# Kernel tuning notes

Hardware: AMD Instinct MI355X
Metric: run time of the kernel (lower is better)

Reference implementation:

```python
import jax, jax.numpy as jnp
import numpy as np

HIDDEN_DIM = 2048
NUM_HEADS = 16
HEAD_DIM = HIDDEN_DIM // NUM_HEADS


def setup_inputs() -> dict:
    key = jax.random.key(0)
    ks = jax.random.split(key, 5)
    B, S, D = 1, 4096, HIDDEN_DIM
    scale = 1.0 / np.sqrt(D)
    x = jax.random.normal(ks[0], (B, S, D), dtype=jnp.float32)
    w_q = jax.random.normal(ks[1], (D, D), dtype=jnp.float32) * scale
    w_k = jax.random.normal(ks[2], (D, D), dtype=jnp.float32) * scale
    w_v = jax.random.normal(ks[3], (D, D), dtype=jnp.float32) * scale
    w_o = jax.random.normal(ks[4], (D, D), dtype=jnp.float32) * scale
    return {"x": x, "w_q": w_q, "w_k": w_k, "w_v": w_v, "w_o": w_o, "causal": 1}


def reference(x, w_q, w_k, w_v, w_o, causal):
    B, S, D = x.shape
    H, Dh = NUM_HEADS, HEAD_DIM
    sm_scale = 1.0 / np.sqrt(Dh)

    # projections (x @ W.T)
    q = jnp.einsum('bsd,ed->bse', x, w_q).reshape(B, S, H, Dh).transpose(0, 2, 1, 3)
    k = jnp.einsum('bsd,ed->bse', x, w_k).reshape(B, S, H, Dh).transpose(0, 2, 1, 3)
    v = jnp.einsum('bsd,ed->bse', x, w_v).reshape(B, S, H, Dh).transpose(0, 2, 1, 3)

    # attention scores [B, H, S, S]; flash online-softmax == standard softmax
    scores = jnp.einsum('bhqd,bhkd->bhqk', q, k) * sm_scale
    if causal:
        qpos = jnp.arange(S)[:, None]
        kpos = jnp.arange(S)[None, :]
        scores = jnp.where(qpos >= kpos, scores, -jnp.inf)
    probs = jax.nn.softmax(scores, axis=-1)
    o = jnp.einsum('bhqk,bhkd->bhqd', probs, v)  # [B, H, S, Dh]
    o = o.transpose(0, 2, 1, 3).reshape(B, S, D)
    return jnp.einsum('bsd,ed->bse', o, w_o)
```

## Files before the change

### kernel.cpp

```cpp
#include <hip/hip_runtime.h>
#include <stdint.h>

typedef __bf16 bf16_t;
typedef __bf16 bf16x8 __attribute__((ext_vector_type(8)));
typedef __bf16 bf16x4 __attribute__((ext_vector_type(4)));
typedef float  f32x4  __attribute__((ext_vector_type(4)));

static constexpr int S  = 4096;
static constexpr int D  = 2048;
static constexpr int H  = 16;
static constexpr int DH = 128;

__device__ __forceinline__ bf16x8 ld8(const bf16_t* p) { return *(const bf16x8*)p; }
__device__ __forceinline__ bf16x8 ld8c(const float* p) {
  const f32x4 a = *(const f32x4*)p;
  const f32x4 b = *(const f32x4*)(p + 4);
  bf16x8 r;
  r[0] = (bf16_t)a[0]; r[1] = (bf16_t)a[1]; r[2] = (bf16_t)a[2]; r[3] = (bf16_t)a[3];
  r[4] = (bf16_t)b[0]; r[5] = (bf16_t)b[1]; r[6] = (bf16_t)b[2]; r[7] = (bf16_t)b[3];
  return r;
}

__device__ __forceinline__ void async_ld16(const bf16_t* g, bf16_t* lds) {
  __builtin_amdgcn_global_load_lds(
      (const __attribute__((address_space(1))) uint32_t*)g,
      (__attribute__((address_space(3))) uint32_t*)lds, 16, 0, 0);
}

__global__ __launch_bounds__(256) void cvt_kernel(
    const float* __restrict__ x,  const float* __restrict__ wq,
    const float* __restrict__ wk, const float* __restrict__ wv,
    const float* __restrict__ wo,
    bf16_t* __restrict__ xb,  bf16_t* __restrict__ wqb,
    bf16_t* __restrict__ wkb, bf16_t* __restrict__ wvb,
    bf16_t* __restrict__ wob) {
  const int z = blockIdx.z;
  const float* src; bf16_t* dst; size_t off = 0;
  if      (z == 0) { src = x;  dst = xb;  off = 0; }
  else if (z == 1) { src = x;  dst = xb;  off = 4194304; }
  else if (z == 2) { src = wq; dst = wqb; }
  else if (z == 3) { src = wk; dst = wkb; }
  else if (z == 4) { src = wv; dst = wvb; }
  else             { src = wo; dst = wob; }
  const size_t i = off + ((size_t)blockIdx.x * 256 + threadIdx.x) * 8;
  *(bf16x8*)(dst + i) = ld8c(src + i);
}

template <typename TC, bool TR>
__device__ __forceinline__ void gemm_async(const bf16_t* __restrict__ A,
                                           const bf16_t* __restrict__ W,
                                           TC* __restrict__ C) {
  constexpr int K  = D;
  constexpr int BK = 32;
  __shared__ __align__(16) bf16_t Ash[128 * BK];
  __shared__ __align__(16) bf16_t Bsh[128 * BK];
  const int tid = threadIdx.x;
  const int w = tid >> 6, lane = tid & 63;
  const int c = lane & 15, g = lane >> 4;
  const int wm = w >> 1, wn = w & 1;
  const int rowBase = blockIdx.y * 128;
  const int colBase = blockIdx.x * 128;

  f32x4 acc[4][4] = {};

  for (int k0 = 0; k0 < K; k0 += BK) {
    __syncthreads();
    #pragma unroll
    for (int r = 0; r < 2; ++r) {
      const int cid = r * 256 + tid;
      const int row = cid >> 2, q = cid & 3;
      async_ld16(A + (size_t)(rowBase + row) * K + k0 + q * 8,
                 Ash + r * 2048 + w * 512);
      async_ld16(W + (size_t)(colBase + row) * K + k0 + q * 8,
                 Bsh + r * 2048 + w * 512);
    }
    __syncthreads();

    bf16x8 af[4], bf[4];
    #pragma unroll
    for (int i = 0; i < 4; ++i) af[i] = ld8(Ash + (wm * 64 + i * 16 + c) * BK + g * 8);
    #pragma unroll
    for (int j = 0; j < 4; ++j) bf[j] = ld8(Bsh + (wn * 64 + j * 16 + c) * BK + g * 8);
    #pragma unroll
    for (int i = 0; i < 4; ++i)
      #pragma unroll
      for (int j = 0; j < 4; ++j)
        acc[i][j] = __builtin_amdgcn_mfma_f32_16x16x32_bf16(af[i], bf[j], acc[i][j], 0, 0, 0);
  }

  #pragma unroll
  for (int i = 0; i < 4; ++i)
    #pragma unroll
    for (int j = 0; j < 4; ++j) {
      if (TR) {
        const int col  = colBase + wn * 64 + j * 16 + c;
        const int row0 = rowBase + wm * 64 + i * 16 + g * 4;
        bf16x4 v;
        #pragma unroll
        for (int r = 0; r < 4; ++r) v[r] = (bf16_t)acc[i][j][r];
        *(bf16x4*)((bf16_t*)C + (size_t)col * S + row0) = v;
      } else {
        #pragma unroll
        for (int r = 0; r < 4; ++r) {
          const int row = rowBase + wm * 64 + i * 16 + g * 4 + r;
          const int col = colBase + wn * 64 + j * 16 + c;
          C[(size_t)row * D + col] = (TC)acc[i][j][r];
        }
      }
    }
}

__global__ __launch_bounds__(256) void qkv_gemm_bf16(
    const bf16_t* __restrict__ X,
    const bf16_t* __restrict__ Wq, const bf16_t* __restrict__ Wk,
    const bf16_t* __restrict__ Wv,
    bf16_t* __restrict__ Qo, bf16_t* __restrict__ Ko, bf16_t* __restrict__ VTo) {
  if (blockIdx.z == 0)      gemm_async<bf16_t, false>(X, Wq, Qo);
  else if (blockIdx.z == 1) gemm_async<bf16_t, false>(X, Wk, Ko);
  else                      gemm_async<bf16_t, true >(X, Wv, VTo);
}

__global__ __launch_bounds__(256) void out_gemm_bf16(
    const bf16_t* __restrict__ A, const bf16_t* __restrict__ W,
    float* __restrict__ C) {
  gemm_async<float, false>(A, W, C);
}

__global__ __launch_bounds__(512, 2) void attn_kernel(
    const bf16_t* __restrict__ Q, const bf16_t* __restrict__ Kb,
    const bf16_t* __restrict__ VTg, bf16_t* __restrict__ O,
    const int* __restrict__ causal_p, int* __restrict__ ctr) {
  __shared__ __align__(16) bf16_t smem[36864];
  bf16_t* const KB0 = smem;
  bf16_t* const VB0 = smem + 16384;
  bf16_t* const Psh = smem + 32768;
  __shared__ int item_s;

  const int tid = threadIdx.x, w = tid >> 6, lane = tid & 63;
  const int c = lane & 15, g = lane >> 4;
  const int wq = w >> 1, wk = w & 1;
  const int causal = causal_p[0];
  constexpr float QS = 0.08838834764831845f * 1.4426950408889634f;

  int knA[2], qK8[2], dVA[2], qV8[2];
  #pragma unroll
  for (int r = 0; r < 2; ++r) {
    const int cid = r * 512 + tid;
    knA[r] = cid >> 4; qK8[r] = (((cid & 15) ^ (knA[r] & 7)) << 3);
    dVA[r] = cid >> 3; qV8[r] = (((cid & 7) ^ (dVA[r] & 7)) << 3);
  }

  bf16_t* const Pw = Psh + w * 512;
  const int psw = (c >> 1) & 3;

  while (true) {
    __syncthreads();
    if (tid == 0) item_s = atomicAdd(ctr, 1);
    __syncthreads();
    const int it = item_s;
    if (it >= 1024) break;
    const int s64 = causal ? (63 - (it >> 4)) : (it >> 4);
    const int h = it & 15;
    const int qrow0 = s64 * 64 + wq * 16;
    const int ktiles = causal ? (s64 + 1) : (S / 64);

    bf16x8 qf[4];
    #pragma unroll
    for (int kf = 0; kf < 4; ++kf) {
      const bf16x8 raw = ld8(Q + (size_t)(qrow0 + c) * D + h * DH + kf * 32 + g * 8);
      bf16x8 sc;
      #pragma unroll
      for (int e = 0; e < 8; ++e) sc[e] = (bf16_t)((float)raw[e] * QS);
      qf[kf] = sc;
    }

    f32x4 o_acc[8] = {};
    float psum = 0.0f;

    #pragma unroll
    for (int r = 0; r < 2; ++r) {
      async_ld16(Kb + (size_t)knA[r] * D + h * DH + qK8[r], KB0 + r * 4096 + w * 512);
      async_ld16(VTg + (size_t)(h * DH + dVA[r]) * S + qV8[r], VB0 + r * 4096 + w * 512);
    }
    __syncthreads();

    int cur = 0;
    for (int kt = 0; kt < ktiles; ++kt) {
      if (kt + 1 < ktiles) {
        const int alt = cur ^ 1;
        #pragma unroll
        for (int r = 0; r < 2; ++r) {
          async_ld16(Kb + (size_t)((kt + 1) * 64 + knA[r]) * D + h * DH + qK8[r],
                     KB0 + alt * 8192 + r * 4096 + w * 512);
          async_ld16(VTg + (size_t)(h * DH + dVA[r]) * S + (kt + 1) * 64 + qV8[r],
                     VB0 + alt * 8192 + r * 4096 + w * 512);
        }
      }

      const bf16_t* const KB = KB0 + cur * 8192;
      const bf16_t* const VB = VB0 + cur * 8192;
      const int kb = kt * 64 + wk * 32;

      const bool active = !causal || (kb <= qrow0 + 15);
      if (active) {
        __builtin_amdgcn_s_setprio(1);
        #pragma unroll
        for (int nf = 0; nf < 2; ++nf) {
          const int rr = wk * 32 + nf * 16 + c;
          f32x4 s = {};
          #pragma unroll
          for (int kf = 0; kf < 4; ++kf) {
            const bf16x8 kk = ld8(KB + rr * 128 + ((((kf << 2) + g) ^ (rr & 7)) << 3));
            s = __builtin_amdgcn_mfma_f32_16x16x32_bf16(kk, qf[kf], s, 0, 0, 0);
          }
          if (causal && (kb + nf * 16 + 15 > qrow0)) {
            #pragma unroll
            for (int r_ = 0; r_ < 4; ++r_)
              if (kb + nf * 16 + g * 4 + r_ > qrow0 + c) s[r_] = -1e30f;
          }
          bf16x4 pq;
          #pragma unroll
          for (int r_ = 0; r_ < 4; ++r_) {
            const float pv = exp2f(s[r_]);
            psum += pv;
            pq[r_] = (bf16_t)pv;
          }
          const int p  = (nf << 1) | (g >> 1);
          const int pp = ((p ^ psw) << 1) | (g & 1);
          *(bf16x4*)(Pw + c * 32 + pp * 4) = pq;
        }

        const bf16x8 pf = ld8(Pw + c * 32 + ((g ^ psw) << 3));
        #pragma unroll
        for (int nf = 0; nf < 8; ++nf) {
          const int dl = nf * 16 + c;
          const bf16x8 vf = ld8(VB + dl * 64 + ((((wk << 2) + g) ^ (dl & 7)) << 3));
          o_acc[nf] = __builtin_amdgcn_mfma_f32_16x16x32_bf16(pf, vf, o_acc[nf], 0, 0, 0);
        }
        __builtin_amdgcn_s_setprio(0);
      }

      __syncthreads();
      cur ^= 1;
    }

    float* const slot = (float*)smem + (size_t)(wq * 64 + lane) * 36;
    if (wk == 1) {
      #pragma unroll
      for (int nf = 0; nf < 8; ++nf) *(f32x4*)(slot + nf * 4) = o_acc[nf];
      slot[32] = psum;
    }
    __syncthreads();
    if (wk == 0) {
      #pragma unroll
      for (int nf = 0; nf < 8; ++nf) o_acc[nf] += *(const f32x4*)(slot + nf * 4);
      psum += slot[32];
      float v = psum;
      v += __shfl_xor(v, 16); v += __shfl_xor(v, 32);
      #pragma unroll
      for (int r_ = 0; r_ < 4; ++r_) {
        const float inv = 1.0f / __shfl(v, g * 4 + r_, 64);
        const int row = qrow0 + g * 4 + r_;
        #pragma unroll
        for (int nf = 0; nf < 8; ++nf)
          O[(size_t)row * D + h * DH + nf * 16 + c] = (bf16_t)(o_acc[nf][r_] * inv);
      }
    }
  }
}

extern "C" void kernel_launch(void* const* d_in, const int* in_sizes, int n_in,
                              void* d_out, int out_size, void* d_ws, size_t ws_size,
                              hipStream_t stream) {
  const float* x  = (const float*)d_in[0];
  const float* wq = (const float*)d_in[1];
  const float* wk = (const float*)d_in[2];
  const float* wv = (const float*)d_in[3];
  const float* wo = (const float*)d_in[4];
  const int* causal = (const int*)d_in[5];
  float* out = (float*)d_out;

  bf16_t* Qb  = (bf16_t*)d_ws;
  bf16_t* Kb  = Qb + (size_t)S * D;
  bf16_t* VTb = Kb + (size_t)S * D;
  bf16_t* Ob  = VTb + (size_t)S * D;
  bf16_t* xb  = Ob + (size_t)S * D;
  bf16_t* wqb = xb + (size_t)S * D;
  bf16_t* wkb = wqb + (size_t)D * D;
  bf16_t* wvb = wkb + (size_t)D * D;
  bf16_t* wob = wvb + (size_t)D * D;
  int*    ctr = (int*)(wob + (size_t)D * D);

  hipMemsetAsync(ctr, 0, sizeof(int), stream);

  dim3 blk(256);
  cvt_kernel<<<dim3(2048, 1, 6), blk, 0, stream>>>(x, wq, wk, wv, wo,
                                                   xb, wqb, wkb, wvb, wob);
  qkv_gemm_bf16<<<dim3(D / 128, S / 128, 3), blk, 0, stream>>>(xb, wqb, wkb, wvb,
                                                               Qb, Kb, VTb);
  attn_kernel<<<dim3(512), dim3(512), 0, stream>>>(Qb, Kb, VTb, Ob, causal, ctr);
  out_gemm_bf16<<<dim3(D / 128, S / 128), blk, 0, stream>>>(Ob, wob, out);
}
```

Baseline: 428.8 us.

## Fuse QKV projections into one GEMM and single-buffer attention for occupancy

The QKV projection becomes one kernel that loads each X tile once and multiplies it against all three weight tiles, so the three accumulator sets share the A-tile loads. The attention kernel drops K/V double buffering to cut shared memory, raises its launch bounds to 4 blocks per CU and launches 768 persistent blocks. The aim is to cut redundant X reads and hide memory latency through occupancy instead of software prefetch. Risks: the fused GEMM holds 192 accumulator floats per thread, which may spill or limit occupancy. It also lacks async prefetch overlap, and attention now waits on each tile load.

```diff
diff --git a/kernel.cpp b/kernel.cpp
--- a/kernel.cpp
+++ b/kernel.cpp
@@ -110,14 +110,73 @@
     }
 }
 
-__global__ __launch_bounds__(256) void qkv_gemm_bf16(
+__global__ __launch_bounds__(256, 2) void qkv_gemm_fused(
     const bf16_t* __restrict__ X,
     const bf16_t* __restrict__ Wq, const bf16_t* __restrict__ Wk,
     const bf16_t* __restrict__ Wv,
     bf16_t* __restrict__ Qo, bf16_t* __restrict__ Ko, bf16_t* __restrict__ VTo) {
-  if (blockIdx.z == 0)      gemm_async<bf16_t, false>(X, Wq, Qo);
-  else if (blockIdx.z == 1) gemm_async<bf16_t, false>(X, Wk, Ko);
-  else                      gemm_async<bf16_t, true >(X, Wv, VTo);
+  constexpr int K  = D;
+  constexpr int BK = 32;
+  __shared__ __align__(16) bf16_t Ash[128 * BK];
+  __shared__ __align__(16) bf16_t Bsh[3][128 * BK];
+  const int tid = threadIdx.x;
+  const int w = tid >> 6, lane = tid & 63;
+  const int c = lane & 15, g = lane >> 4;
+  const int wm = w >> 1, wn = w & 1;
+  const int rowBase = blockIdx.y * 128;
+  const int colBase = blockIdx.x * 128;
+
+  f32x4 acc[3][4][4] = {};
+
+  for (int k0 = 0; k0 < K; k0 += BK) {
+    __syncthreads();
+    #pragma unroll
+    for (int r = 0; r < 2; ++r) {
+      const int cid = r * 256 + tid;
+      const int row = cid >> 2, q = cid & 3;
+      const size_t aoff = (size_t)(rowBase + row) * K + k0 + q * 8;
+      const size_t boff = (size_t)(colBase + row) * K + k0 + q * 8;
+      async_ld16(X  + aoff, Ash    + r * 2048 + w * 512);
+      async_ld16(Wq + boff, Bsh[0] + r * 2048 + w * 512);
+      async_ld16(Wk + boff, Bsh[1] + r * 2048 + w * 512);
+      async_ld16(Wv + boff, Bsh[2] + r * 2048 + w * 512);
+    }
+    __syncthreads();
+
+    bf16x8 af[4];
+    #pragma unroll
+    for (int i = 0; i < 4; ++i) af[i] = ld8(Ash + (wm * 64 + i * 16 + c) * BK + g * 8);
+    #pragma unroll
+    for (int m = 0; m < 3; ++m) {
+      bf16x8 bf[4];
+      #pragma unroll
+      for (int j = 0; j < 4; ++j) bf[j] = ld8(Bsh[m] + (wn * 64 + j * 16 + c) * BK + g * 8);
+      #pragma unroll
+      for (int i = 0; i < 4; ++i)
+        #pragma unroll
+        for (int j = 0; j < 4; ++j)
+          acc[m][i][j] = __builtin_amdgcn_mfma_f32_16x16x32_bf16(af[i], bf[j], acc[m][i][j], 0, 0, 0);
+    }
+  }
+
+  #pragma unroll
+  for (int i = 0; i < 4; ++i)
+    #pragma unroll
+    for (int j = 0; j < 4; ++j) {
+      #pragma unroll
+      for (int r = 0; r < 4; ++r) {
+        const int row = rowBase + wm * 64 + i * 16 + g * 4 + r;
+        const int col = colBase + wn * 64 + j * 16 + c;
+        Qo[(size_t)row * D + col] = (bf16_t)acc[0][i][j][r];
+        Ko[(size_t)row * D + col] = (bf16_t)acc[1][i][j][r];
+      }
+      const int colv  = colBase + wn * 64 + j * 16 + c;
+      const int row0v = rowBase + wm * 64 + i * 16 + g * 4;
+      bf16x4 v;
+      #pragma unroll
+      for (int r = 0; r < 4; ++r) v[r] = (bf16_t)acc[2][i][j][r];
+      *(bf16x4*)(VTo + (size_t)colv * S + row0v) = v;
+    }
 }
 
 __global__ __launch_bounds__(256) void out_gemm_bf16(
@@ -126,15 +185,15 @@
   gemm_async<float, false>(A, W, C);
 }
 
-__global__ __launch_bounds__(512, 2) void attn_kernel(
+__global__ __launch_bounds__(512, 4) void attn_kernel(
     const bf16_t* __restrict__ Q, const bf16_t* __restrict__ Kb,
     const bf16_t* __restrict__ VTg, bf16_t* __restrict__ O,
     const int* __restrict__ causal_p, int* __restrict__ ctr) {
-  __shared__ __align__(16) bf16_t smem[36864];
-  bf16_t* const KB0 = smem;
-  bf16_t* const VB0 = smem + 16384;
-  bf16_t* const Psh = smem + 32768;
-  __shared__ int item_s;
+  __shared__ __align__(16) bf16_t smem[20480];
+  bf16_t* const KB  = smem;
+  bf16_t* const VB  = smem + 8192;
+  bf16_t* const Psh = smem + 16384;
+  int* const item_sp = (int*)(smem + 20478);
 
   const int tid = threadIdx.x, w = tid >> 6, lane = tid & 63;
   const int c = lane & 15, g = lane >> 4;
@@ -154,16 +213,23 @@
   const int psw = (c >> 1) & 3;
 
   while (true) {
-    __syncthreads();
-    if (tid == 0) item_s = atomicAdd(ctr, 1);
-    __syncthreads();
-    const int it = item_s;
+    if (tid == 0) *item_sp = atomicAdd(ctr, 1);
+    __syncthreads();
+    const int it = *item_sp;
     if (it >= 1024) break;
     const int s64 = causal ? (63 - (it >> 4)) : (it >> 4);
     const int h = it & 15;
     const int qrow0 = s64 * 64 + wq * 16;
     const int ktiles = causal ? (s64 + 1) : (S / 64);
 
+    const bf16_t* kSrc[2];
+    const bf16_t* vSrc[2];
+    #pragma unroll
+    for (int r = 0; r < 2; ++r) {
+      kSrc[r] = Kb + (size_t)knA[r] * D + h * DH + qK8[r];
+      vSrc[r] = VTg + (size_t)(h * DH + dVA[r]) * S + qV8[r];
+    }
+
     bf16x8 qf[4];
     #pragma unroll
     for (int kf = 0; kf < 4; ++kf) {
@@ -177,30 +243,17 @@
     f32x4 o_acc[8] = {};
     float psum = 0.0f;
 
-    #pragma unroll
-    for (int r = 0; r < 2; ++r) {
-      async_ld16(Kb + (size_t)knA[r] * D + h * DH + qK8[r], KB0 + r * 4096 + w * 512);
-      async_ld16(VTg + (size_t)(h * DH + dVA[r]) * S + qV8[r], VB0 + r * 4096 + w * 512);
-    }
-    __syncthreads();
-
-    int cur = 0;
     for (int kt = 0; kt < ktiles; ++kt) {
-      if (kt + 1 < ktiles) {
-        const int alt = cur ^ 1;
-        #pragma unroll
-        for (int r = 0; r < 2; ++r) {
-          async_ld16(Kb + (size_t)((kt + 1) * 64 + knA[r]) * D + h * DH + qK8[r],
-                     KB0 + alt * 8192 + r * 4096 + w * 512);
-          async_ld16(VTg + (size_t)(h * DH + dVA[r]) * S + (kt + 1) * 64 + qV8[r],
-                     VB0 + alt * 8192 + r * 4096 + w * 512);
-        }
-      }
-
-      const bf16_t* const KB = KB0 + cur * 8192;
-      const bf16_t* const VB = VB0 + cur * 8192;
+      #pragma unroll
+      for (int r = 0; r < 2; ++r) {
+        async_ld16(kSrc[r], KB + r * 4096 + w * 512);
+        async_ld16(vSrc[r], VB + r * 4096 + w * 512);
+        kSrc[r] += (size_t)64 * D;
+        vSrc[r] += 64;
+      }
+      __syncthreads();
+
       const int kb = kt * 64 + wk * 32;
-
       const bool active = !causal || (kb <= qrow0 + 15);
       if (active) {
         __builtin_amdgcn_s_setprio(1);
@@ -241,7 +294,6 @@
       }
 
       __syncthreads();
-      cur ^= 1;
     }
 
     float* const slot = (float*)smem + (size_t)(wq * 64 + lane) * 36;
@@ -296,8 +348,8 @@
   dim3 blk(256);
   cvt_kernel<<<dim3(2048, 1, 6), blk, 0, stream>>>(x, wq, wk, wv, wo,
                                                    xb, wqb, wkb, wvb, wob);
-  qkv_gemm_bf16<<<dim3(D / 128, S / 128, 3), blk, 0, stream>>>(xb, wqb, wkb, wvb,
-                                                               Qb, Kb, VTb);
-  attn_kernel<<<dim3(512), dim3(512), 0, stream>>>(Qb, Kb, VTb, Ob, causal, ctr);
+  qkv_gemm_fused<<<dim3(D / 128, S / 128), blk, 0, stream>>>(xb, wqb, wkb, wvb,
+                                                             Qb, Kb, VTb);
+  attn_kernel<<<dim3(768), dim3(512), 0, stream>>>(Qb, Kb, VTb, Ob, causal, ctr);
   out_gemm_bf16<<<dim3(D / 128, S / 128), blk, 0, stream>>>(Ob, wob, out);
 }
```

Result: faster. 414.9 us (-3.2%).
